# Kernel optimization log

Hardware: AMD Instinct MI355X
Metric: run time of the kernel (lower is better)

## Reference

```python
import jax, jax.numpy as jnp
import numpy as np
import math

D_MODEL = 1024
NUM_HEADS = 16
D_K = D_MODEL // NUM_HEADS
MAX_SEQ_LEN = 2048
THETA = 10000.0
BATCH = 2
SEQ = 2048


def setup_inputs() -> dict:
    key = jax.random.key(0)
    ks = jax.random.split(key, 5)
    std = math.sqrt(2.0 / (D_MODEL + D_MODEL))
    def w(k):
        return jnp.clip(std * jax.random.normal(k, (D_MODEL, D_MODEL), dtype=jnp.float32), -3 * std, 3 * std)
    return {
        "x": jax.random.normal(ks[0], (BATCH, SEQ, D_MODEL), dtype=jnp.float32),
        "token_positions": jnp.arange(SEQ, dtype=jnp.int32),
        "Wq": w(ks[1]),
        "Wk": w(ks[2]),
        "Wv": w(ks[3]),
        "Wo": w(ks[4]),
    }


def _rope_tables():
    inv_freq = 1.0 / THETA ** (jnp.arange(0, D_K, 2, dtype=jnp.float32) / D_K)  # [d_k/2]
    positions = jnp.arange(MAX_SEQ_LEN, dtype=jnp.float32)[:, None]             # [max_seq, 1]
    angles = positions * inv_freq                                               # [max_seq, d_k/2]
    return jnp.cos(angles), jnp.sin(angles)


def _apply_rope(x, cos, sin):
    # x: [..., seq, d_k]; cos/sin: [seq, d_k/2] (broadcast over leading dims)
    x1, x2 = x[..., ::2], x[..., 1::2]
    r1 = x1 * cos - x2 * sin
    r2 = x1 * sin + x2 * cos
    return jnp.stack((r1, r2), axis=-1).reshape(x.shape)


def reference(x, token_positions, Wq, Wk, Wv, Wo):
    B, S, D = x.shape
    def proj(W):
        y = jnp.einsum('bsd,od->bso', x, W)
        return y.reshape(B, S, NUM_HEADS, D_K).transpose(0, 2, 1, 3)  # [B,H,S,dk]
    q, k, v = proj(Wq), proj(Wk), proj(Wv)

    cos_t, sin_t = _rope_tables()
    cos, sin = cos_t[token_positions], sin_t[token_positions]  # [S, d_k/2]
    q = _apply_rope(q, cos, sin)
    k = _apply_rope(k, cos, sin)

    scores = jnp.einsum('bhqd,bhkd->bhqk', q, k) / math.sqrt(D_K)
    causal = jnp.tril(jnp.ones((S, S), dtype=bool))
    scores = jnp.where(causal, scores, -jnp.inf)
    attn = jax.nn.softmax(scores, axis=-1)
    out = jnp.einsum('bhqk,bhkd->bhqd', attn, v)
    out = out.transpose(0, 2, 1, 3).reshape(B, S, D)
    return jnp.einsum('bsd,od->bso', out, Wo)
```

## Files before the change

### kernel.cpp

```cpp
#include <hip/hip_runtime.h>
#include <hip/hip_bf16.h>


typedef __attribute__((ext_vector_type(8))) short short8;
typedef __attribute__((ext_vector_type(4))) float floatx4;

static __device__ __forceinline__ unsigned short f2bf(float f) {
  __hip_bfloat16 h = __float2bfloat16(f);
  return *(unsigned short*)&h;
}

static __device__ __forceinline__ void gl2lds16(const unsigned short* g,
                                                unsigned short* l) {
  __builtin_amdgcn_global_load_lds(
      (const __attribute__((address_space(1))) void*)g,
      (__attribute__((address_space(3))) void*)l, 16, 0, 0);
}

__global__ __launch_bounds__(256) void cvt_all(
    const float4* __restrict__ x,  const float4* __restrict__ wq,
    const float4* __restrict__ wk, const float4* __restrict__ wv,
    const float4* __restrict__ wo,
    ushort4* __restrict__ xb,  ushort4* __restrict__ wqb,
    ushort4* __restrict__ wkb, ushort4* __restrict__ wvb,
    ushort4* __restrict__ wob) {
  int t = blockIdx.y;
  const float4* s = (t == 0) ? x : (t == 1) ? wq : (t == 2) ? wk : (t == 3) ? wv : wo;
  ushort4* d = (t == 0) ? xb : (t == 1) ? wqb : (t == 2) ? wkb : (t == 3) ? wvb : wob;
  int n4 = (t == 0) ? 1048576 : 262144;
  int i = blockIdx.x * 256 + threadIdx.x;
  if (i < n4) {
    float4 v = s[i];
    ushort4 o;
    o.x = f2bf(v.x); o.y = f2bf(v.y); o.z = f2bf(v.z); o.w = f2bf(v.w);
    d[i] = o;
  }
}

__global__ void rope_tables(const int* __restrict__ tokpos,
                            float* __restrict__ ctab, float* __restrict__ stab) {
  int idx = blockIdx.x * 256 + threadIdx.x;
  int s = idx >> 5;
  int i = idx & 31;
  float inv = expf(-9.210340371976184f * (float)(2 * i) / 64.0f);
  float ang = (float)tokpos[s] * inv;
  ctab[idx] = cosf(ang);
  stab[idx] = sinf(ang);
}

#define GEMM128_BODY(Aptr, Wptr, m0, n0)                                        \
  __shared__ __align__(16) unsigned short lA[128 * 64];                         \
  __shared__ __align__(16) unsigned short lB[128 * 64];                         \
  int tid = threadIdx.x;                                                        \
  int wave = tid >> 6, lane = tid & 63;                                         \
  int wm = wave >> 1, wn = wave & 1;                                            \
  int l15 = lane & 15, quad = lane >> 4;                                        \
  int srow = wave * 32 + (lane >> 3);                   \
  int sch = lane & 7;                                   \
  int fsw = l15 & 7;                                 \
  floatx4 acc[4][4];                                                            \
  _Pragma("unroll") for (int m = 0; m < 4; ++m)                                 \
      _Pragma("unroll") for (int n = 0; n < 4; ++n)                             \
          acc[m][n] = (floatx4){0.f, 0.f, 0.f, 0.f};                            \
  for (int kt = 0; kt < 16; ++kt) {                                             \
    _Pragma("unroll") for (int p = 0; p < 4; ++p) {                             \
      int r = srow + p * 8;                                                     \
      int g = sch ^ (r & 7);                                                    \
      gl2lds16(Aptr + (size_t)(m0 + r) * 1024 + kt * 64 + g * 8,                \
               lA + (wave * 32 + p * 8) * 64);                                  \
      gl2lds16(Wptr + (size_t)(n0 + r) * 1024 + kt * 64 + g * 8,                \
               lB + (wave * 32 + p * 8) * 64);                                  \
    }                                                                           \
    __syncthreads();                                                            \
    _Pragma("unroll") for (int ks = 0; ks < 2; ++ks) {                          \
      short8 af[4], bf[4];                                                      \
      _Pragma("unroll") for (int m = 0; m < 4; ++m)                             \
          af[m] = *(const short8*)(lA + (wm * 64 + m * 16 + l15) * 64 +         \
                                   (((ks * 4 + quad) ^ fsw) * 8));              \
      _Pragma("unroll") for (int n = 0; n < 4; ++n)                             \
          bf[n] = *(const short8*)(lB + (wn * 64 + n * 16 + l15) * 64 +         \
                                   (((ks * 4 + quad) ^ fsw) * 8));              \
      _Pragma("unroll") for (int m = 0; m < 4; ++m)                             \
          _Pragma("unroll") for (int n = 0; n < 4; ++n)                         \
              acc[m][n] = __builtin_amdgcn_mfma_f32_16x16x32_bf16(              \
                  af[m], bf[n], acc[m][n], 0, 0, 0);                            \
    }                                                                           \
    __syncthreads();                                                            \
  }

__global__ __launch_bounds__(256) void qkv_mfma(
    const unsigned short* __restrict__ X,
    const unsigned short* __restrict__ Wq,
    const unsigned short* __restrict__ Wk,
    const unsigned short* __restrict__ Wv,
    const float* __restrict__ ctab, const float* __restrict__ stab,
    unsigned short* __restrict__ Qo, unsigned short* __restrict__ Ko,
    unsigned short* __restrict__ Vo) {
  int mat = blockIdx.z;
  const unsigned short* W = (mat == 0) ? Wq : ((mat == 1) ? Wk : Wv);
  unsigned short* Out = (mat == 0) ? Qo : ((mat == 1) ? Ko : Vo);
  int m0 = blockIdx.x * 128, n0 = blockIdx.y * 128;

  GEMM128_BODY(X, W, m0, n0)

#pragma unroll
  for (int n = 0; n < 4; ++n) {
    int col = n0 + wn * 64 + n * 16 + l15;
    int h = col >> 6;
    int d = col & 63;
    int pi = d >> 1;
    bool odd = (d & 1) != 0;
    size_t hb = (size_t)h * 2048 * 64;
#pragma unroll
    for (int m = 0; m < 4; ++m) {
      int row0 = m0 + wm * 64 + m * 16 + quad * 4;
      int b = row0 >> 11;
      int s0 = row0 & 2047;
      size_t base = (size_t)b * 16 * 2048 * 64 + hb;
      if (mat == 2) {
        ushort4 pv;
        pv.x = f2bf(acc[m][n][0]);
        pv.y = f2bf(acc[m][n][1]);
        pv.z = f2bf(acc[m][n][2]);
        pv.w = f2bf(acc[m][n][3]);
        *(ushort4*)(Out + base + (size_t)d * 2048 + s0) = pv;
      } else {
#pragma unroll
        for (int i = 0; i < 4; ++i) {
          int s = s0 + i;
          float v = acc[m][n][i];
          float p = __shfl_xor(v, 1);
          float c = ctab[s * 32 + pi];
          float sn = stab[s * 32 + pi];
          float res = odd ? fmaf(p, sn, v * c) : fmaf(v, c, -p * sn);
          if (mat == 0) res *= 0.125f;
          Out[base + (size_t)s * 64 + d] = f2bf(res);
        }
      }
    }
  }
}

__global__ __launch_bounds__(256) void oproj_mfma(
    const unsigned short* __restrict__ A, const unsigned short* __restrict__ Wo,
    float* __restrict__ Out) {
  int m0 = blockIdx.x * 128, n0 = blockIdx.y * 128;

  GEMM128_BODY(A, Wo, m0, n0)

#pragma unroll
  for (int m = 0; m < 4; ++m) {
#pragma unroll
    for (int n = 0; n < 4; ++n) {
      int col = n0 + wn * 64 + n * 16 + l15;
#pragma unroll
      for (int i = 0; i < 4; ++i) {
        int row = m0 + wm * 64 + m * 16 + quad * 4 + i;
        Out[(size_t)row * 1024 + col] = acc[m][n][i];
      }
    }
  }
}

#define LKS 72

__global__ __launch_bounds__(256) void attn_flash(
    const unsigned short* __restrict__ Q, const unsigned short* __restrict__ K,
    const unsigned short* __restrict__ Vt, unsigned short* __restrict__ Oc) {
  __shared__ unsigned short lK[64 * LKS];
  __shared__ unsigned short lV[64 * LKS];
  __shared__ unsigned short lP[4][16 * LKS];

  int tid = threadIdx.x;
  int wave = tid >> 6, lane = tid & 63;
  int l15 = lane & 15, quad = lane >> 4;

  int xb_ = blockIdx.x;
  int yb_ = blockIdx.y;
  int jb = yb_ >> 3, ib = yb_ & 7;
  int qtile;
  if (jb == 0)      qtile = xb_;
  else if (jb == 1) qtile = 31 - xb_;
  else if (jb == 2) qtile = (15 - xb_) & 31;
  else              qtile = (16 + xb_) & 31;
  int bh = ib * 4 + jb;

  size_t base = (size_t)bh * 2048 * 64;
  int qbase = qtile * 64;

  const unsigned short* qrow = Q + base + (size_t)(qbase + wave * 16 + l15) * 64;
  short8 qb0 = *(const short8*)(qrow + quad * 8);
  short8 qb1 = *(const short8*)(qrow + 32 + quad * 8);

  floatx4 o[4];
  float m_i = -1e30f, l_i = 0.f;
#pragma unroll
  for (int n = 0; n < 4; ++n) o[n] = (floatx4){0.f, 0.f, 0.f, 0.f};

  int r0 = tid >> 3, e0 = (tid & 7) * 8;
  int r1 = r0 + 32;

  const unsigned short* kp = K + base;
  const unsigned short* vp = Vt + base;
  short8 pk0 = *(const short8*)(kp + r0 * 64 + e0);
  short8 pk1 = *(const short8*)(kp + r1 * 64 + e0);
  short8 pv0 = *(const short8*)(vp + (size_t)r0 * 2048 + e0);
  short8 pv1 = *(const short8*)(vp + (size_t)r1 * 2048 + e0);

  for (int kt = 0; kt <= qtile; ++kt) {
    __syncthreads();
    *(short8*)(lK + r0 * LKS + e0) = pk0;
    *(short8*)(lK + r1 * LKS + e0) = pk1;
    *(short8*)(lV + r0 * LKS + e0) = pv0;
    *(short8*)(lV + r1 * LKS + e0) = pv1;
    __syncthreads();

    if (kt < qtile) {
      const unsigned short* kn = K + base + (size_t)(kt + 1) * 64 * 64;
      const unsigned short* vn = Vt + base + (kt + 1) * 64;
      pk0 = *(const short8*)(kn + r0 * 64 + e0);
      pk1 = *(const short8*)(kn + r1 * 64 + e0);
      pv0 = *(const short8*)(vn + (size_t)r0 * 2048 + e0);
      pv1 = *(const short8*)(vn + (size_t)r1 * 2048 + e0);
    }

    float sc[4][4];
#pragma unroll
    for (int sub = 0; sub < 4; ++sub) {
      const unsigned short* kr = lK + (sub * 16 + l15) * LKS + quad * 8;
      short8 a0 = *(const short8*)(kr);
      short8 a1 = *(const short8*)(kr + 32);
      floatx4 s = {0.f, 0.f, 0.f, 0.f};
      s = __builtin_amdgcn_mfma_f32_16x16x32_bf16(a0, qb0, s, 0, 0, 0);
      s = __builtin_amdgcn_mfma_f32_16x16x32_bf16(a1, qb1, s, 0, 0, 0);
#pragma unroll
      for (int i = 0; i < 4; ++i) sc[sub][i] = s[i];
    }

    if (kt == qtile) {
      int qin = wave * 16 + l15;
#pragma unroll
      for (int sub = 0; sub < 4; ++sub)
#pragma unroll
        for (int i = 0; i < 4; ++i)
          if (sub * 16 + quad * 4 + i > qin) sc[sub][i] = -1e30f;
    }

    float mb = sc[0][0];
#pragma unroll
    for (int sub = 0; sub < 4; ++sub)
#pragma unroll
      for (int i = 0; i < 4; ++i) mb = fmaxf(mb, sc[sub][i]);
    mb = fmaxf(mb, __shfl_xor(mb, 16));
    mb = fmaxf(mb, __shfl_xor(mb, 32));

    float mn = fmaxf(m_i, mb);
    float al = __expf(m_i - mn);
    m_i = mn;
    float rs = 0.f;
#pragma unroll
    for (int sub = 0; sub < 4; ++sub)
#pragma unroll
      for (int i = 0; i < 4; ++i) {
        float p = __expf(sc[sub][i] - mn);
        sc[sub][i] = p;
        rs += p;
      }
    rs += __shfl_xor(rs, 16);
    rs += __shfl_xor(rs, 32);
    l_i = l_i * al + rs;

#pragma unroll
    for (int n = 0; n < 4; ++n) {
      o[n][0] *= al; o[n][1] *= al; o[n][2] *= al; o[n][3] *= al;
    }

    unsigned short* pw = lP[wave];
#pragma unroll
    for (int sub = 0; sub < 4; ++sub) {
      ushort4 pq;
      pq.x = f2bf(sc[sub][0]); pq.y = f2bf(sc[sub][1]);
      pq.z = f2bf(sc[sub][2]); pq.w = f2bf(sc[sub][3]);
      *(ushort4*)(pw + l15 * LKS + sub * 16 + quad * 4) = pq;
    }

    const unsigned short* pr = pw + l15 * LKS + quad * 8;
    short8 pa0 = *(const short8*)(pr);
    short8 pa1 = *(const short8*)(pr + 32);

#pragma unroll
    for (int n = 0; n < 4; ++n) {
      const unsigned short* vr = lV + (n * 16 + l15) * LKS + quad * 8;
      short8 vb0 = *(const short8*)(vr);
      short8 vb1 = *(const short8*)(vr + 32);
      o[n] = __builtin_amdgcn_mfma_f32_16x16x32_bf16(vb0, pa0, o[n], 0, 0, 0);
      o[n] = __builtin_amdgcn_mfma_f32_16x16x32_bf16(vb1, pa1, o[n], 0, 0, 0);
    }
  }

  int b = bh >> 4, h = bh & 15;
  float inv = 1.f / l_i;
  int s = qbase + wave * 16 + l15;
  size_t orow = (size_t)(b * 2048 + s) * 1024 + h * 64;
#pragma unroll
  for (int n = 0; n < 4; ++n) {
    ushort4 ov;
    ov.x = f2bf(o[n][0] * inv);
    ov.y = f2bf(o[n][1] * inv);
    ov.z = f2bf(o[n][2] * inv);
    ov.w = f2bf(o[n][3] * inv);
    *(ushort4*)(Oc + orow + n * 16 + quad * 4) = ov;
  }
}

extern "C" void kernel_launch(void* const* d_in, const int* in_sizes, int n_in,
                              void* d_out, int out_size, void* d_ws, size_t ws_size,
                              hipStream_t stream) {
  const float* x  = (const float*)d_in[0];
  const int* tokpos = (const int*)d_in[1];
  const float* Wq = (const float*)d_in[2];
  const float* Wk = (const float*)d_in[3];
  const float* Wv = (const float*)d_in[4];
  const float* Wo = (const float*)d_in[5];
  float* out = (float*)d_out;

  float* ws = (float*)d_ws;
  float* ctab = ws;
  float* stab = ctab + 65536;
  unsigned short* u = (unsigned short*)(stab + 65536);
  unsigned short* Qb  = u;
  unsigned short* Kb  = Qb + 4194304;
  unsigned short* Vb  = Kb + 4194304;
  unsigned short* Oc  = Vb + 4194304;
  unsigned short* xb  = Oc + 4194304;
  unsigned short* Wqb = xb + 4194304;
  unsigned short* Wkb = Wqb + 1048576;
  unsigned short* Wvb = Wkb + 1048576;
  unsigned short* Wob = Wvb + 1048576;

  cvt_all<<<dim3(4096, 5), 256, 0, stream>>>(
      (const float4*)x, (const float4*)Wq, (const float4*)Wk,
      (const float4*)Wv, (const float4*)Wo,
      (ushort4*)xb, (ushort4*)Wqb, (ushort4*)Wkb, (ushort4*)Wvb, (ushort4*)Wob);

  rope_tables<<<256, 256, 0, stream>>>(tokpos, ctab, stab);
  qkv_mfma<<<dim3(32, 8, 3), 256, 0, stream>>>(
      xb, Wqb, Wkb, Wvb, ctab, stab, Qb, Kb, Vb);
  attn_flash<<<dim3(32, 32), 256, 0, stream>>>(Qb, Kb, Vb, Oc);
  oproj_mfma<<<dim3(32, 8), 256, 0, stream>>>(Oc, Wob, out);
}
```

Measured before the change: 201.1 us.

## Fuse rope tables into convert kernel, swizzle attention LDS, use exp2 softmax

Folds the RoPE table computation into the conversion kernel as an extra grid row, which removes one kernel launch. The attention K/V shared-memory tiles drop the padded stride in favour of an XOR-swizzled 64-element layout, cutting LDS use while trying to avoid bank conflicts. The Q scale now includes log2(e), so softmax can use exp2f in place of __expf. The cvt grid grows to 6 rows, and most blocks in the new rope row exit at once without doing work.

```diff
diff --git a/kernel.cpp b/kernel.cpp
--- a/kernel.cpp
+++ b/kernel.cpp
@@ -23,29 +23,30 @@
     const float4* __restrict__ wo,
     ushort4* __restrict__ xb,  ushort4* __restrict__ wqb,
     ushort4* __restrict__ wkb, ushort4* __restrict__ wvb,
-    ushort4* __restrict__ wob) {
+    ushort4* __restrict__ wob,
+    const int* __restrict__ tokpos,
+    float* __restrict__ ctab, float* __restrict__ stab) {
   int t = blockIdx.y;
+  int i = blockIdx.x * 256 + threadIdx.x;
+  if (t == 5) {
+    if (i < 65536) {
+      int s = i >> 5, f = i & 31;
+      float inv = expf(-9.210340371976184f * (float)(2 * f) / 64.0f);
+      float ang = (float)tokpos[s] * inv;
+      ctab[i] = cosf(ang);
+      stab[i] = sinf(ang);
+    }
+    return;
+  }
   const float4* s = (t == 0) ? x : (t == 1) ? wq : (t == 2) ? wk : (t == 3) ? wv : wo;
   ushort4* d = (t == 0) ? xb : (t == 1) ? wqb : (t == 2) ? wkb : (t == 3) ? wvb : wob;
   int n4 = (t == 0) ? 1048576 : 262144;
-  int i = blockIdx.x * 256 + threadIdx.x;
   if (i < n4) {
     float4 v = s[i];
     ushort4 o;
     o.x = f2bf(v.x); o.y = f2bf(v.y); o.z = f2bf(v.z); o.w = f2bf(v.w);
     d[i] = o;
   }
-}
-
-__global__ void rope_tables(const int* __restrict__ tokpos,
-                            float* __restrict__ ctab, float* __restrict__ stab) {
-  int idx = blockIdx.x * 256 + threadIdx.x;
-  int s = idx >> 5;
-  int i = idx & 31;
-  float inv = expf(-9.210340371976184f * (float)(2 * i) / 64.0f);
-  float ang = (float)tokpos[s] * inv;
-  ctab[idx] = cosf(ang);
-  stab[idx] = sinf(ang);
 }
 
 #define GEMM128_BODY(Aptr, Wptr, m0, n0)                                        \
@@ -133,7 +134,7 @@
           float c = ctab[s * 32 + pi];
           float sn = stab[s * 32 + pi];
           float res = odd ? fmaf(p, sn, v * c) : fmaf(v, c, -p * sn);
-          if (mat == 0) res *= 0.125f;
+          if (mat == 0) res *= 0.1803368801111204f;
           Out[base + (size_t)s * 64 + d] = f2bf(res);
         }
       }
@@ -162,14 +163,14 @@
   }
 }
 
-#define LKS 72
+#define LPS 72
 
 __global__ __launch_bounds__(256) void attn_flash(
     const unsigned short* __restrict__ Q, const unsigned short* __restrict__ K,
     const unsigned short* __restrict__ Vt, unsigned short* __restrict__ Oc) {
-  __shared__ unsigned short lK[64 * LKS];
-  __shared__ unsigned short lV[64 * LKS];
-  __shared__ unsigned short lP[4][16 * LKS];
+  __shared__ __align__(16) unsigned short lK[64 * 64];
+  __shared__ __align__(16) unsigned short lV[64 * 64];
+  __shared__ unsigned short lP[4][16 * LPS];
 
   int tid = threadIdx.x;
   int wave = tid >> 6, lane = tid & 63;
@@ -197,8 +198,13 @@
 #pragma unroll
   for (int n = 0; n < 4; ++n) o[n] = (floatx4){0.f, 0.f, 0.f, 0.f};
 
-  int r0 = tid >> 3, e0 = (tid & 7) * 8;
+  int r0 = tid >> 3, g = tid & 7;
   int r1 = r0 + 32;
+  int e0 = g * 8;
+  int sl = (g ^ (r0 & 7)) * 8;
+  int fsw = l15 & 7;
+  int c0 = (quad ^ fsw) * 8;
+  int c1 = ((quad + 4) ^ fsw) * 8;
 
   const unsigned short* kp = K + base;
   const unsigned short* vp = Vt + base;
@@ -209,10 +215,10 @@
 
   for (int kt = 0; kt <= qtile; ++kt) {
     __syncthreads();
-    *(short8*)(lK + r0 * LKS + e0) = pk0;
-    *(short8*)(lK + r1 * LKS + e0) = pk1;
-    *(short8*)(lV + r0 * LKS + e0) = pv0;
-    *(short8*)(lV + r1 * LKS + e0) = pv1;
+    *(short8*)(lK + r0 * 64 + sl) = pk0;
+    *(short8*)(lK + r1 * 64 + sl) = pk1;
+    *(short8*)(lV + r0 * 64 + sl) = pv0;
+    *(short8*)(lV + r1 * 64 + sl) = pv1;
     __syncthreads();
 
     if (kt < qtile) {
@@ -227,9 +233,9 @@
     float sc[4][4];
 #pragma unroll
     for (int sub = 0; sub < 4; ++sub) {
-      const unsigned short* kr = lK + (sub * 16 + l15) * LKS + quad * 8;
-      short8 a0 = *(const short8*)(kr);
-      short8 a1 = *(const short8*)(kr + 32);
+      const unsigned short* kr = lK + (sub * 16 + l15) * 64;
+      short8 a0 = *(const short8*)(kr + c0);
+      short8 a1 = *(const short8*)(kr + c1);
       floatx4 s = {0.f, 0.f, 0.f, 0.f};
       s = __builtin_amdgcn_mfma_f32_16x16x32_bf16(a0, qb0, s, 0, 0, 0);
       s = __builtin_amdgcn_mfma_f32_16x16x32_bf16(a1, qb1, s, 0, 0, 0);
@@ -255,14 +261,14 @@
     mb = fmaxf(mb, __shfl_xor(mb, 32));
 
     float mn = fmaxf(m_i, mb);
-    float al = __expf(m_i - mn);
+    float al = exp2f(m_i - mn);
     m_i = mn;
     float rs = 0.f;
 #pragma unroll
     for (int sub = 0; sub < 4; ++sub)
 #pragma unroll
       for (int i = 0; i < 4; ++i) {
-        float p = __expf(sc[sub][i] - mn);
+        float p = exp2f(sc[sub][i] - mn);
         sc[sub][i] = p;
         rs += p;
       }
@@ -281,18 +287,18 @@
       ushort4 pq;
       pq.x = f2bf(sc[sub][0]); pq.y = f2bf(sc[sub][1]);
       pq.z = f2bf(sc[sub][2]); pq.w = f2bf(sc[sub][3]);
-      *(ushort4*)(pw + l15 * LKS + sub * 16 + quad * 4) = pq;
-    }
-
-    const unsigned short* pr = pw + l15 * LKS + quad * 8;
+      *(ushort4*)(pw + l15 * LPS + sub * 16 + quad * 4) = pq;
+    }
+
+    const unsigned short* pr = pw + l15 * LPS + quad * 8;
     short8 pa0 = *(const short8*)(pr);
     short8 pa1 = *(const short8*)(pr + 32);
 
 #pragma unroll
     for (int n = 0; n < 4; ++n) {
-      const unsigned short* vr = lV + (n * 16 + l15) * LKS + quad * 8;
-      short8 vb0 = *(const short8*)(vr);
-      short8 vb1 = *(const short8*)(vr + 32);
+      const unsigned short* vr = lV + (n * 16 + l15) * 64;
+      short8 vb0 = *(const short8*)(vr + c0);
+      short8 vb1 = *(const short8*)(vr + c1);
       o[n] = __builtin_amdgcn_mfma_f32_16x16x32_bf16(vb0, pa0, o[n], 0, 0, 0);
       o[n] = __builtin_amdgcn_mfma_f32_16x16x32_bf16(vb1, pa1, o[n], 0, 0, 0);
     }
@@ -338,12 +344,12 @@
   unsigned short* Wvb = Wkb + 1048576;
   unsigned short* Wob = Wvb + 1048576;
 
-  cvt_all<<<dim3(4096, 5), 256, 0, stream>>>(
+  cvt_all<<<dim3(4096, 6), 256, 0, stream>>>(
       (const float4*)x, (const float4*)Wq, (const float4*)Wk,
       (const float4*)Wv, (const float4*)Wo,
-      (ushort4*)xb, (ushort4*)Wqb, (ushort4*)Wkb, (ushort4*)Wvb, (ushort4*)Wob);
-
-  rope_tables<<<256, 256, 0, stream>>>(tokpos, ctab, stab);
+      (ushort4*)xb, (ushort4*)Wqb, (ushort4*)Wkb, (ushort4*)Wvb, (ushort4*)Wob,
+      tokpos, ctab, stab);
+
   qkv_mfma<<<dim3(32, 8, 3), 256, 0, stream>>>(
       xb, Wqb, Wkb, Wvb, ctab, stab, Qb, Kb, Vb);
   attn_flash<<<dim3(32, 32), 256, 0, stream>>>(Qb, Kb, Vb, Oc);
```

Result: no change. 203.3 us (+1.1%).
